# Optimization experiments

Hardware: AMD Instinct MI355X
Metric: run time of the kernel (lower is better)

The kernel has to match this reference:

```python
import jax, jax.numpy as jnp
import numpy as np

NU, NI, E, C = 100000, 50000, 500000, 128
TAU = 1.0
TEMP = 0.1

def _cos(a, b):
    # torch F.cosine_similarity: dot / (max(|a|,eps) * max(|b|,eps)), eps=1e-8
    na = jnp.maximum(jnp.linalg.norm(a, axis=-1), 1e-8)
    nb = jnp.maximum(jnp.linalg.norm(b, axis=-1), 1e-8)
    return jnp.sum(a * b, axis=-1) / (na * nb)

def _ln(x, g, b):
    m = jnp.mean(x, axis=-1, keepdims=True)
    v = jnp.var(x, axis=-1, keepdims=True)
    return (x - m) * jax.lax.rsqrt(v + 1e-5) * g + b

def _gumbel_hard(logits, u, tau):
    # F.gumbel_softmax(hard=True) with straight-through estimator; u ~ U(0,1) supplied as input
    g = -jnp.log(-jnp.log(u * (1.0 - 2e-6) + 1e-6))
    y = jax.nn.softmax((logits + g) / tau, axis=-1)
    hard = jax.nn.one_hot(jnp.argmax(y, axis=-1), y.shape[-1], dtype=y.dtype)
    return jax.lax.stop_gradient(hard - y) + y

def _forward(x_user, x_item, item_pop, u_user, u_item,
             Wu_proj, bu_proj, Wi_proj, bi_proj,
             Wu_enc, bu_enc, Wu_act, bu_act,
             Wi_enc, bi_enc, Wi_fair, bi_fair,
             Wl_ui, Wr_ui, b_ui, Wl_iu, Wr_iu, b_iu,
             ln_u_g, ln_u_b, ln_i_g, ln_i_b,
             edge_ui, edge_iu, user_neg_idx, item_neg_idx):
    hu = x_user @ Wu_proj + bu_proj          # [NU, C] user_proj
    hi = x_item @ Wi_proj + bi_proj          # [NI, C] item_proj
    # FairUserNet (fair_score head output is discarded in original; omitted)
    eu = jax.nn.relu(hu @ Wu_enc + bu_enc)
    action_logits = eu @ Wu_act + bu_act     # [NU, 2]
    # FairItemNet
    ei = jax.nn.relu(hi @ Wi_enc + bi_enc)
    pop = jax.nn.sigmoid(item_pop)[:, None]
    item_logits = jnp.concatenate([ei, pop], axis=-1) @ Wi_fair + bi_fair  # [NI, 2]
    user_probs = _gumbel_hard(action_logits, u_user, TAU)[:, 0]
    item_probs = _gumbel_hard(item_logits, u_item, TAU)[:, 0]  # WeightedSAGEConv discards edge weights
    del item_probs
    # structural contrastive loss over positive edges
    src, dst = edge_ui[0], edge_ui[1]
    ue, ie = hu[src], hi[dst]                # [E, C] gathers
    pos = _cos(ue, ie)
    neg = _cos(ue, hi[item_neg_idx]) + _cos(hu[user_neg_idx], ie)
    pe = jnp.exp(pos / TEMP)
    ne = jnp.exp(neg / TEMP)
    struct_loss = -jnp.mean(jnp.log(pe / (pe + ne)))
    # 3 hetero SAGE layers (2 hidden + final); aggr='add' (sum), lin_l bias, lin_r no bias
    isrc, idst = edge_iu[0], edge_iu[1]
    for l in range(3):
        agg_i = jax.ops.segment_sum(hu[src], dst, num_segments=NI)    # user -> item
        agg_u = jax.ops.segment_sum(hi[isrc], idst, num_segments=NU)  # item -> user
        new_i = agg_i @ Wl_ui[l] + b_ui[l] + hi @ Wr_ui[l]
        new_u = agg_u @ Wl_iu[l] + b_iu[l] + hu @ Wr_iu[l]
        if l < 2:  # LayerNorm + dropout(eval=identity) only on the 2 hidden layers
            new_u = _ln(new_u, ln_u_g[l], ln_u_b[l])
            new_i = _ln(new_i, ln_i_g[l], ln_i_b[l])
        hu, hi = new_u, new_i
    return hu, hi, struct_loss, user_probs

def setup_inputs():
    key = jax.random.key(0)
    ks = iter(jax.random.split(key, 64))
    def N(shape, s=1.0):
        return jax.random.normal(next(ks), shape, jnp.float32) * s
    def U(shape):
        return jax.random.uniform(next(ks), shape, dtype=jnp.float32)
    def I(shape, hi):
        return jax.random.randint(next(ks), shape, 0, hi, dtype=jnp.int32)
    w = 0.05
    users = I((E,), NU)
    items = I((E,), NI)
    return {
        'x_user': N((NU, C)), 'x_item': N((NI, C)),
        'item_pop': N((NI,)),
        'u_user': U((NU, 2)), 'u_item': U((NI, 2)),
        'Wu_proj': N((C, C), w), 'bu_proj': N((C,), w),
        'Wi_proj': N((C, C), w), 'bi_proj': N((C,), w),
        'Wu_enc': N((C, C), w), 'bu_enc': N((C,), w),
        'Wu_act': N((C, 2), w), 'bu_act': N((2,), w),
        'Wi_enc': N((C, C), w), 'bi_enc': N((C,), w),
        'Wi_fair': N((C + 1, 2), w), 'bi_fair': N((2,), w),
        'Wl_ui': N((3, C, C), w), 'Wr_ui': N((3, C, C), w), 'b_ui': N((3, C), w),
        'Wl_iu': N((3, C, C), w), 'Wr_iu': N((3, C, C), w), 'b_iu': N((3, C), w),
        'ln_u_g': jnp.ones((2, C), jnp.float32), 'ln_u_b': jnp.zeros((2, C), jnp.float32),
        'ln_i_g': jnp.ones((2, C), jnp.float32), 'ln_i_b': jnp.zeros((2, C), jnp.float32),
        'edge_ui': jnp.stack([users, items]),
        'edge_iu': jnp.stack([items, users]),
        'sensitive_attr': I((NU,), 2),
        'user_neg_idx': I((E,), NU),
        'item_neg_idx': I((E,), NI),
    }

def reference(x_user, x_item, item_pop, u_user, u_item,
              Wu_proj, bu_proj, Wi_proj, bi_proj,
              Wu_enc, bu_enc, Wu_act, bu_act,
              Wi_enc, bi_enc, Wi_fair, bi_fair,
              Wl_ui, Wr_ui, b_ui, Wl_iu, Wr_iu, b_iu,
              ln_u_g, ln_u_b, ln_i_g, ln_i_b,
              edge_ui, edge_iu, sensitive_attr, user_neg_idx, item_neg_idx):
    del sensitive_attr  # only feeds the discarded user fair_score head / .item() side effects
    return _forward(x_user, x_item, item_pop, u_user, u_item,
                    Wu_proj, bu_proj, Wi_proj, bi_proj,
                    Wu_enc, bu_enc, Wu_act, bu_act,
                    Wi_enc, bi_enc, Wi_fair, bi_fair,
                    Wl_ui, Wr_ui, b_ui, Wl_iu, Wr_iu, b_iu,
                    ln_u_g, ln_u_b, ln_i_g, ln_i_b,
                    edge_ui, edge_iu, user_neg_idx, item_neg_idx)
```

## Files before the change

kernel.cpp:

```cpp
#include <hip/hip_runtime.h>

#define NUU 100000
#define NII 50000
#define NEDGE 500000
#define NROWS (NII + NUU)

typedef float f32x4 __attribute__((ext_vector_type(4)));
typedef short bf16x8 __attribute__((ext_vector_type(8)));
typedef _Float16 half8v __attribute__((ext_vector_type(8)));
typedef _Float16 half4v __attribute__((ext_vector_type(4)));

struct GemmP {
    const float* A1; const unsigned short* Wh1; const unsigned short* Wl1;
    const float* A2; const unsigned short* Wh2; const unsigned short* Wl2;
    const float* bias; const float* lg; const float* lb;
    float* out; _Float16* out16; float* nrm; int M; int mode;
};

__global__ __launch_bounds__(256, 2)
void gemm_dual(GemmP P0, GemmP P1, int gb0,
               const float* __restrict__ pw, const float* __restrict__ pb,
               const float* __restrict__ pu, float* __restrict__ pout)
{
    const bool sel = (blockIdx.x >= gb0);
    const GemmP P = sel ? P1 : P0;
    const int bi = sel ? (int)blockIdx.x - gb0 : (int)blockIdx.x;
    const int tid = threadIdx.x;
    const int l  = tid & 63;
    const int w  = tid >> 6;
    const int lm = l & 15;
    const int lk = l >> 4;
    const int rowb = bi * 256 + w * 64;

    f32x4 acc[4][8];
#pragma unroll
    for (int mt = 0; mt < 4; ++mt)
#pragma unroll
        for (int nt = 0; nt < 8; ++nt) acc[mt][nt] = (f32x4){0.f, 0.f, 0.f, 0.f};

    const int nmat = (P.A2 != nullptr) ? 2 : 1;
    for (int m = 0; m < nmat; ++m) {
        const float* A = m ? P.A2 : P.A1;
        const unsigned short* Wh = m ? P.Wh2 : P.Wh1;
        const unsigned short* Wl = m ? P.Wl2 : P.Wl1;
#pragma unroll
        for (int kt = 0; kt < 4; ++kt) {
            bf16x8 ah[4], al[4];
#pragma unroll
            for (int mt = 0; mt < 4; ++mt) {
                int row = rowb + mt * 16 + lm;
                int rowc = row < P.M ? row : P.M - 1;
                const float* ap = A + (size_t)rowc * 128 + kt * 32 + lk * 8;
                float4 f0 = *(const float4*)ap;
                float4 f1 = *(const float4*)(ap + 4);
                float a8[8] = {f0.x, f0.y, f0.z, f0.w, f1.x, f1.y, f1.z, f1.w};
                union { bf16x8 v; unsigned int u[4]; } H, L;
#pragma unroll
                for (int p = 0; p < 4; ++p) {
                    unsigned int u0 = __float_as_uint(a8[2 * p]);
                    unsigned int u1 = __float_as_uint(a8[2 * p + 1]);
                    H.u[p] = (u0 >> 16) | (u1 & 0xffff0000u);
                    float l0 = a8[2 * p]     - __uint_as_float(u0 & 0xffff0000u);
                    float l1 = a8[2 * p + 1] - __uint_as_float(u1 & 0xffff0000u);
                    L.u[p] = (__float_as_uint(l0) >> 16) | (__float_as_uint(l1) & 0xffff0000u);
                }
                ah[mt] = H.v;
                al[mt] = L.v;
            }
#pragma unroll
            for (int h = 0; h < 2; ++h) {
                bf16x8 bh[4], bl[4];
#pragma unroll
                for (int q = 0; q < 4; ++q) {
                    size_t fo = (size_t)((kt * 8 + h * 4 + q) * 64 + l) * 8;
                    bh[q] = *(const bf16x8*)(Wh + fo);
                    bl[q] = *(const bf16x8*)(Wl + fo);
                }
#pragma unroll
                for (int mt = 0; mt < 4; ++mt)
#pragma unroll
                    for (int q = 0; q < 4; ++q) {
                        int nt = h * 4 + q;
                        acc[mt][nt] = __builtin_amdgcn_mfma_f32_16x16x32_bf16(bh[q], ah[mt], acc[mt][nt], 0, 0, 0);
                        acc[mt][nt] = __builtin_amdgcn_mfma_f32_16x16x32_bf16(bl[q], ah[mt], acc[mt][nt], 0, 0, 0);
                        acc[mt][nt] = __builtin_amdgcn_mfma_f32_16x16x32_bf16(bh[q], al[mt], acc[mt][nt], 0, 0, 0);
                    }
            }
        }
    }

    f32x4 bv[8];
#pragma unroll
    for (int nt = 0; nt < 8; ++nt)
        bv[nt] = *(const f32x4*)(P.bias + nt * 16 + lk * 4);

#pragma unroll
    for (int mt = 0; mt < 4; ++mt) {
        int row = rowb + mt * 16 + lm;
        bool valid = row < P.M;
        float v[8][4];
#pragma unroll
        for (int nt = 0; nt < 8; ++nt)
#pragma unroll
            for (int i = 0; i < 4; ++i) v[nt][i] = acc[mt][nt][i] + bv[nt][i];
        if (P.mode == 1) {
#pragma unroll
            for (int nt = 0; nt < 8; ++nt)
#pragma unroll
                for (int i = 0; i < 4; ++i) v[nt][i] = fmaxf(v[nt][i], 0.f);
        } else if (P.mode == 2) {
            float s = 0.f, sq = 0.f;
#pragma unroll
            for (int nt = 0; nt < 8; ++nt)
#pragma unroll
                for (int i = 0; i < 4; ++i) { s += v[nt][i]; sq += v[nt][i] * v[nt][i]; }
            s  += __shfl_xor(s, 16, 64);  s  += __shfl_xor(s, 32, 64);
            sq += __shfl_xor(sq, 16, 64); sq += __shfl_xor(sq, 32, 64);
            float mean = s * (1.f / 128.f);
            float var  = sq * (1.f / 128.f) - mean * mean;
            float inv  = rsqrtf(var + 1e-5f);
#pragma unroll
            for (int nt = 0; nt < 8; ++nt) {
                f32x4 lg = *(const f32x4*)(P.lg + nt * 16 + lk * 4);
                f32x4 lb = *(const f32x4*)(P.lb + nt * 16 + lk * 4);
#pragma unroll
                for (int i = 0; i < 4; ++i) v[nt][i] = (v[nt][i] - mean) * inv * lg[i] + lb[i];
            }
        }
        if (pout != nullptr) {
            float q0 = 0.f, q1 = 0.f;
#pragma unroll
            for (int nt = 0; nt < 8; ++nt) {
                const float* pp = pw + (size_t)(nt * 16 + lk * 4) * 2;
                f32x4 pa = *(const f32x4*)pp;
                f32x4 pc = *(const f32x4*)(pp + 4);
                q0 += v[nt][0] * pa[0] + v[nt][1] * pa[2] + v[nt][2] * pc[0] + v[nt][3] * pc[2];
                q1 += v[nt][0] * pa[1] + v[nt][1] * pa[3] + v[nt][2] * pc[1] + v[nt][3] * pc[3];
            }
            q0 += __shfl_xor(q0, 16, 64); q0 += __shfl_xor(q0, 32, 64);
            q1 += __shfl_xor(q1, 16, 64); q1 += __shfl_xor(q1, 32, 64);
            if (lk == 0 && valid) {
                float l0 = q0 + pb[0], l1 = q1 + pb[1];
                float u0 = pu[2 * row], u1 = pu[2 * row + 1];
                float g0 = -logf(-logf(u0 * (1.f - 2e-6f) + 1e-6f));
                float g1 = -logf(-logf(u1 * (1.f - 2e-6f) + 1e-6f));
                float z0 = l0 + g0, z1 = l1 + g1;
                float mz = fmaxf(z0, z1);
                float e0 = expf(z0 - mz), e1 = expf(z1 - mz);
                float y0 = e0 / (e0 + e1);
                pout[row] = (z0 >= z1) ? ((1.f - y0) + y0) : 0.f;
            }
        }
        if (P.nrm != nullptr) {
            float sq = 0.f;
#pragma unroll
            for (int nt = 0; nt < 8; ++nt)
#pragma unroll
                for (int i = 0; i < 4; ++i) sq += v[nt][i] * v[nt][i];
            sq += __shfl_xor(sq, 16, 64); sq += __shfl_xor(sq, 32, 64);
            if (lk == 0 && valid) P.nrm[row] = fmaxf(sqrtf(sq), 1e-8f);
        }
        if (valid) {
            if (P.out != nullptr) {
#pragma unroll
                for (int nt = 0; nt < 8; ++nt)
                    *(float4*)(P.out + (size_t)row * 128 + nt * 16 + lk * 4) =
                        make_float4(v[nt][0], v[nt][1], v[nt][2], v[nt][3]);
            }
            if (P.out16 != nullptr) {
#pragma unroll
                for (int nt = 0; nt < 8; ++nt) {
                    half4v h;
#pragma unroll
                    for (int i = 0; i < 4; ++i) h[i] = (_Float16)v[nt][i];
                    *(half4v*)(P.out16 + (size_t)row * 128 + nt * 16 + lk * 4) = h;
                }
            }
        }
    }
}

struct WSrc { const float* p[7]; };
__global__ void wsplit_k(WSrc S, unsigned short* __restrict__ wout)
{
    int gid = blockIdx.x * 256 + threadIdx.x;
    if (gid >= 15 * 16384) return;
    int m = gid >> 14;
    int idx = gid & 16383;
    int k = idx >> 7, n = idx & 127;
    const float* src;
    if (m == 0) src = S.p[0];
    else if (m == 1) src = S.p[1];
    else if (m == 2) src = S.p[2];
    else if (m < 6)  src = S.p[3] + (size_t)(m - 3) * 16384;
    else if (m < 9)  src = S.p[4] + (size_t)(m - 6) * 16384;
    else if (m < 12) src = S.p[5] + (size_t)(m - 9) * 16384;
    else             src = S.p[6] + (size_t)(m - 12) * 16384;
    float wv = src[idx];
    unsigned int u = __float_as_uint(wv);
    unsigned short hi = (unsigned short)(u >> 16);
    float lof = wv - __uint_as_float(u & 0xffff0000u);
    unsigned short lo = (unsigned short)(__float_as_uint(lof) >> 16);
    int kt = k >> 5, kr = k & 31;
    int dst = ((kt * 8 + (n >> 4)) * 64 + ((kr >> 3) * 16 + (n & 15))) * 8 + (kr & 7);
    unsigned short* wm = wout + (size_t)m * 32768;
    wm[dst] = hi;
    wm[dst + 16384] = lo;
}

__global__ void loss_k(const _Float16* __restrict__ hu16, const _Float16* __restrict__ hi16,
                       const float* __restrict__ nu, const float* __restrict__ ni,
                       const int* __restrict__ src, const int* __restrict__ dst,
                       const int* __restrict__ uneg, const int* __restrict__ ineg,
                       float* __restrict__ loss, int ne)
{
    __shared__ float ls[4];
    int lane = threadIdx.x & 63;
    int q = lane >> 4;
    int c8 = (lane & 15) * 8;
    int wib = threadIdx.x >> 6;
    int gw = (blockIdx.x * blockDim.x + threadIdx.x) >> 6;
    int nw = (gridDim.x * blockDim.x) >> 6;
    float part = 0.f;
    for (int eb = gw; eb < ne / 4; eb += nw) {
        int e = eb * 4 + q;
        int s = src[e], d = dst[e], un = uneg[e], in_ = ineg[e];
        half8v a = *(const half8v*)(hu16 + (size_t)s * 128 + c8);
        half8v b = *(const half8v*)(hi16 + (size_t)d * 128 + c8);
        half8v c = *(const half8v*)(hi16 + (size_t)in_ * 128 + c8);
        half8v dd = *(const half8v*)(hu16 + (size_t)un * 128 + c8);
        float p_sd = 0.f, p_sn = 0.f, p_nd = 0.f;
#pragma unroll
        for (int j = 0; j < 8; ++j) {
            float af = (float)a[j], bf = (float)b[j];
            p_sd += af * bf;
            p_sn += af * (float)c[j];
            p_nd += (float)dd[j] * bf;
        }
#pragma unroll
        for (int m = 1; m < 16; m <<= 1) {
            p_sd += __shfl_xor(p_sd, m, 64);
            p_sn += __shfl_xor(p_sn, m, 64);
            p_nd += __shfl_xor(p_nd, m, 64);
        }
        if ((lane & 15) == 0) {
            float pos = p_sd / (nu[s] * ni[d]);
            float neg = p_sn / (nu[s] * ni[in_]) + p_nd / (nu[un] * ni[d]);
            float pe = expf(pos * 10.f);
            float nex = expf(neg * 10.f);
            part += -logf(pe / (pe + nex));
        }
    }
    part += __shfl_xor(part, 16, 64);
    part += __shfl_xor(part, 32, 64);
    if (lane == 0) ls[wib] = part;
    __syncthreads();
    if (threadIdx.x == 0)
        atomicAdd(loss, (ls[0] + ls[1] + ls[2] + ls[3]) * (1.f / 500000.f));
}

__global__ void hist2_k(const int* __restrict__ ui_dst, const int* __restrict__ iu_dst,
                        int* __restrict__ deg)
{
    int e = blockIdx.x * blockDim.x + threadIdx.x;
    if (e < NEDGE) atomicAdd(&deg[ui_dst[e]], 1);
    else if (e < 2 * NEDGE) atomicAdd(&deg[NII + iu_dst[e - NEDGE]], 1);
}

__global__ void scan_part_k(const int* __restrict__ in, int* __restrict__ part, int N)
{
    __shared__ int wsum[4];
    int base = blockIdx.x * 1024 + threadIdx.x * 4;
    int s = 0;
    if (base + 3 < N) {
        int4 v = *(const int4*)(in + base);
        s = v.x + v.y + v.z + v.w;
    } else {
#pragma unroll
        for (int j = 0; j < 4; ++j) if (base + j < N) s += in[base + j];
    }
#pragma unroll
    for (int m = 1; m < 64; m <<= 1) s += __shfl_xor(s, m, 64);
    if ((threadIdx.x & 63) == 0) wsum[threadIdx.x >> 6] = s;
    __syncthreads();
    if (threadIdx.x == 0) part[blockIdx.x] = wsum[0] + wsum[1] + wsum[2] + wsum[3];
}

__global__ void scan_top_k(int* __restrict__ p, int nb)
{
    __shared__ int sm[256];
    int t = threadIdx.x;
    int v = (t < nb) ? p[t] : 0;
    sm[t] = v;
    __syncthreads();
    for (int o = 1; o < 256; o <<= 1) {
        int x = (t >= o) ? sm[t - o] : 0;
        __syncthreads();
        sm[t] += x;
        __syncthreads();
    }
    if (t < nb) p[t] = sm[t] - v;
}

__global__ void scan_final_k(const int* __restrict__ in, const int* __restrict__ part,
                             int* __restrict__ out, int N, int total)
{
    __shared__ int wtot[4];
    int tid = threadIdx.x;
    int lane = tid & 63, wid = tid >> 6;
    int base = blockIdx.x * 1024 + tid * 4;
    int v[4] = {0, 0, 0, 0};
    bool full = (base + 3 < N);
    if (full) {
        int4 q = *(const int4*)(in + base);
        v[0] = q.x; v[1] = q.y; v[2] = q.z; v[3] = q.w;
    } else {
#pragma unroll
        for (int j = 0; j < 4; ++j) if (base + j < N) v[j] = in[base + j];
    }
    int s = v[0] + v[1] + v[2] + v[3];
    int incl = s;
#pragma unroll
    for (int o = 1; o < 64; o <<= 1) {
        int n = __shfl_up(incl, o, 64);
        if (lane >= o) incl += n;
    }
    if (lane == 63) wtot[wid] = incl;
    __syncthreads();
    int woff = 0;
    for (int w2 = 0; w2 < wid; ++w2) woff += wtot[w2];
    int run = part[blockIdx.x] + woff + incl - s;
    if (full) {
        int4 o4 = make_int4(run, run + v[0], run + v[0] + v[1], run + v[0] + v[1] + v[2]);
        *(int4*)(out + base) = o4;
    } else {
#pragma unroll
        for (int j = 0; j < 4; ++j) {
            if (base + j < N) { out[base + j] = run; run += v[j]; }
        }
    }
    if (blockIdx.x == 0 && tid == 0) out[N] = total;
}

__global__ void fill2_k(const int* __restrict__ ui_dst, const int* __restrict__ ui_src,
                        const int* __restrict__ iu_dst, const int* __restrict__ iu_src,
                        const int* __restrict__ rowstart, int* __restrict__ cursor,
                        int* __restrict__ elist)
{
    int e = blockIdx.x * blockDim.x + threadIdx.x;
    if (e < NEDGE) {
        int d = ui_dst[e];
        int p = atomicAdd(&cursor[d], 1);
        elist[rowstart[d] + p] = ui_src[e];
    } else if (e < 2 * NEDGE) {
        int d = NII + iu_dst[e - NEDGE];
        int p = atomicAdd(&cursor[d], 1);
        elist[rowstart[d] + p] = iu_src[e - NEDGE];
    }
}

__global__ void agg_dual(const _Float16* __restrict__ hu16, const _Float16* __restrict__ hi16,
                         const int* __restrict__ rowstart, const int* __restrict__ elist,
                         float* __restrict__ hi_n, float* __restrict__ hu_n)
{
    int gt = blockIdx.x * blockDim.x + threadIdx.x;
    int w = gt >> 6, lane = gt & 63;
    if (w >= NROWS) return;
    const _Float16* src;
    float* dst;
    if (w < NII) { src = hu16; dst = hi_n + (size_t)w * 128; }
    else         { src = hi16; dst = hu_n + (size_t)(w - NII) * 128; }
    int q = lane >> 4;
    int c8 = (lane & 15) * 8;
    int s0 = rowstart[w], s1 = rowstart[w + 1];
    float a[8] = {0.f, 0.f, 0.f, 0.f, 0.f, 0.f, 0.f, 0.f};
    for (int e = s0 + q; e < s1; e += 4) {
        int s = elist[e];
        half8v v = *(const half8v*)(src + (size_t)s * 128 + c8);
#pragma unroll
        for (int j = 0; j < 8; ++j) a[j] += (float)v[j];
    }
#pragma unroll
    for (int j = 0; j < 8; ++j) {
        a[j] += __shfl_xor(a[j], 16, 64);
        a[j] += __shfl_xor(a[j], 32, 64);
    }
    if (lane < 16) {
        *(float4*)(dst + c8)     = make_float4(a[0], a[1], a[2], a[3]);
        *(float4*)(dst + c8 + 4) = make_float4(a[4], a[5], a[6], a[7]);
    }
}

extern "C" void kernel_launch(void* const* d_in, const int* in_sizes, int n_in,
                              void* d_out, int out_size, void* d_ws, size_t ws_size,
                              hipStream_t stream)
{
    const float* x_user  = (const float*)d_in[0];
    const float* x_item  = (const float*)d_in[1];
    const float* u_user  = (const float*)d_in[3];
    const float* Wu_proj = (const float*)d_in[5];
    const float* bu_proj = (const float*)d_in[6];
    const float* Wi_proj = (const float*)d_in[7];
    const float* bi_proj = (const float*)d_in[8];
    const float* Wu_enc  = (const float*)d_in[9];
    const float* bu_enc  = (const float*)d_in[10];
    const float* Wu_act  = (const float*)d_in[11];
    const float* bu_act  = (const float*)d_in[12];
    const float* Wl_ui = (const float*)d_in[17];
    const float* Wr_ui = (const float*)d_in[18];
    const float* b_ui  = (const float*)d_in[19];
    const float* Wl_iu = (const float*)d_in[20];
    const float* Wr_iu = (const float*)d_in[21];
    const float* b_iu  = (const float*)d_in[22];
    const float* ln_u_g = (const float*)d_in[23];
    const float* ln_u_b = (const float*)d_in[24];
    const float* ln_i_g = (const float*)d_in[25];
    const float* ln_i_b = (const float*)d_in[26];
    const int* edge_ui  = (const int*)d_in[27];
    const int* edge_iu  = (const int*)d_in[28];
    const int* user_neg = (const int*)d_in[30];
    const int* item_neg = (const int*)d_in[31];

    float* out = (float*)d_out;
    float* out_hu   = out;
    float* out_hi   = out + (size_t)NUU * 128;
    float* out_loss = out + 19200000;
    float* out_prob = out + 19200001;

    float* hu0  = (float*)d_ws;
    float* hi0  = hu0 + (size_t)NUU * 128;
    float* nu   = hi0 + (size_t)NII * 128;
    float* ni   = nu + NUU;
    int* ip   = (int*)(ni + NII);
    int* rs   = ip;  ip += NROWS + 16;
    int* cur  = ip;  ip += NROWS;
    int* el   = ip;  ip += 2 * NEDGE;
    int* pt   = ip;  ip += 160;
    unsigned short* wsp = (unsigned short*)ip;
    _Float16* hu16 = (_Float16*)(wsp + 15 * 32768);
    _Float16* hi16 = hu16 + (size_t)NUU * 128;

    const int* ui_src = edge_ui;
    const int* ui_dst = edge_ui + NEDGE;
    const int* iu_src = edge_iu;
    const int* iu_dst = edge_iu + NEDGE;

    const int GB_U = (NUU + 255) / 256, GB_I = (NII + 255) / 256;
    const int PB = (NROWS + 1023) / 1024;

    WSrc ws7 = {{Wu_proj, Wi_proj, Wu_enc, Wl_ui, Wr_ui, Wl_iu, Wr_iu}};
    wsplit_k<<<(15 * 16384 + 255) / 256, 256, 0, stream>>>(ws7, wsp);
    unsigned short* wm[15];
    for (int m = 0; m < 15; ++m) wm[m] = wsp + (size_t)m * 32768;

    GemmP pu_ = {x_user, wm[0], wm[0] + 16384, nullptr, nullptr, nullptr,
                 bu_proj, nullptr, nullptr, hu0, hu16, nu, NUU, 0};
    GemmP pi_ = {x_item, wm[1], wm[1] + 16384, nullptr, nullptr, nullptr,
                 bi_proj, nullptr, nullptr, hi0, hi16, ni, NII, 0};
    gemm_dual<<<GB_U + GB_I, 256, 0, stream>>>(pu_, pi_, GB_U, nullptr, nullptr, nullptr, nullptr);
    GemmP pe_ = {hu0, wm[2], wm[2] + 16384, nullptr, nullptr, nullptr,
                 bu_enc, nullptr, nullptr, nullptr, nullptr, nullptr, NUU, 1};
    gemm_dual<<<GB_U, 256, 0, stream>>>(pe_, pe_, GB_U, Wu_act, bu_act, u_user, out_prob);
    hipMemsetAsync(out_loss, 0, 4, stream);
    loss_k<<<2048, 256, 0, stream>>>(hu16, hi16, nu, ni, ui_src, ui_dst, user_neg, item_neg, out_loss, NEDGE);
    hipMemsetAsync(cur, 0, (size_t)NROWS * 4, stream);
    hist2_k<<<(2 * NEDGE + 255) / 256, 256, 0, stream>>>(ui_dst, iu_dst, cur);
    scan_part_k<<<PB, 256, 0, stream>>>(cur, pt, NROWS);
    scan_top_k<<<1, 256, 0, stream>>>(pt, PB);
    scan_final_k<<<PB, 256, 0, stream>>>(cur, pt, rs, NROWS, 2 * NEDGE);
    hipMemsetAsync(cur, 0, (size_t)NROWS * 4, stream);
    fill2_k<<<(2 * NEDGE + 255) / 256, 256, 0, stream>>>(ui_dst, ui_src, iu_dst, iu_src, rs, cur, el);

    float* hu_c = hu0; float* hi_c = hi0;
    float* hu_n = out_hu; float* hi_n = out_hi;
    for (int l = 0; l < 3; ++l) {
        int mode = (l < 2) ? 2 : 0;
        agg_dual<<<NROWS / 4, 256, 0, stream>>>(hu16, hi16, rs, el, hi_n, hu_n);
        GemmP li_ = {hi_n, wm[3 + l], wm[3 + l] + 16384, hi_c, wm[6 + l], wm[6 + l] + 16384,
                     b_ui + l * 128, ln_i_g + (l < 2 ? l : 0) * 128, ln_i_b + (l < 2 ? l : 0) * 128,
                     hi_n, (l < 2) ? hi16 : nullptr, nullptr, NII, mode};
        GemmP lu_ = {hu_n, wm[9 + l], wm[9 + l] + 16384, hu_c, wm[12 + l], wm[12 + l] + 16384,
                     b_iu + l * 128, ln_u_g + (l < 2 ? l : 0) * 128, ln_u_b + (l < 2 ? l : 0) * 128,
                     hu_n, (l < 2) ? hu16 : nullptr, nullptr, NUU, mode};
        gemm_dual<<<GB_I + GB_U, 256, 0, stream>>>(li_, lu_, GB_I, nullptr, nullptr, nullptr, nullptr);
        float* t;
        t = hu_c; hu_c = hu_n; hu_n = t;
        t = hi_c; hi_c = hi_n; hi_n = t;
    }
}
```

Measured before the change: 879.3 us.

## Keep SAGE layer activations in fp16 and raise gemm occupancy bound

The aggregation kernel now writes fp16 neighbour sums. The layer GEMMs read both the aggregate and the self term from fp16 buffers, and fp32 results are written only for the final layer's outputs. This cuts memory traffic for the intermediate [N,128] tensors and drops a workspace buffer. The GEMM launch bound is also raised from 2 to 3 blocks per CU. That trades register budget for occupancy and could cause spills. The self term and sums now carry fp16 rounding, which risks accuracy.

```diff
diff --git a/kernel.cpp b/kernel.cpp
--- a/kernel.cpp
+++ b/kernel.cpp
@@ -11,13 +11,13 @@
 typedef _Float16 half4v __attribute__((ext_vector_type(4)));
 
 struct GemmP {
-    const float* A1; const unsigned short* Wh1; const unsigned short* Wl1;
-    const float* A2; const unsigned short* Wh2; const unsigned short* Wl2;
+    const void* A1; const unsigned short* Wh1; const unsigned short* Wl1;
+    const void* A2; const unsigned short* Wh2; const unsigned short* Wl2;
     const float* bias; const float* lg; const float* lb;
-    float* out; _Float16* out16; float* nrm; int M; int mode;
+    float* out; _Float16* out16; float* nrm; int M; int mode; int a16;
 };
 
-__global__ __launch_bounds__(256, 2)
+__global__ __launch_bounds__(256, 3)
 void gemm_dual(GemmP P0, GemmP P1, int gb0,
                const float* __restrict__ pw, const float* __restrict__ pb,
                const float* __restrict__ pu, float* __restrict__ pout)
@@ -40,7 +40,7 @@
 
     const int nmat = (P.A2 != nullptr) ? 2 : 1;
     for (int m = 0; m < nmat; ++m) {
-        const float* A = m ? P.A2 : P.A1;
+        const void* A = m ? P.A2 : P.A1;
         const unsigned short* Wh = m ? P.Wh2 : P.Wh1;
         const unsigned short* Wl = m ? P.Wl2 : P.Wl1;
 #pragma unroll
@@ -50,10 +50,19 @@
             for (int mt = 0; mt < 4; ++mt) {
                 int row = rowb + mt * 16 + lm;
                 int rowc = row < P.M ? row : P.M - 1;
-                const float* ap = A + (size_t)rowc * 128 + kt * 32 + lk * 8;
-                float4 f0 = *(const float4*)ap;
-                float4 f1 = *(const float4*)(ap + 4);
-                float a8[8] = {f0.x, f0.y, f0.z, f0.w, f1.x, f1.y, f1.z, f1.w};
+                float a8[8];
+                if (P.a16) {
+                    const _Float16* ap = (const _Float16*)A + (size_t)rowc * 128 + kt * 32 + lk * 8;
+                    half8v hv = *(const half8v*)ap;
+#pragma unroll
+                    for (int j = 0; j < 8; ++j) a8[j] = (float)hv[j];
+                } else {
+                    const float* ap = (const float*)A + (size_t)rowc * 128 + kt * 32 + lk * 8;
+                    float4 f0 = *(const float4*)ap;
+                    float4 f1 = *(const float4*)(ap + 4);
+                    a8[0] = f0.x; a8[1] = f0.y; a8[2] = f0.z; a8[3] = f0.w;
+                    a8[4] = f1.x; a8[5] = f1.y; a8[6] = f1.z; a8[7] = f1.w;
+                }
                 union { bf16x8 v; unsigned int u[4]; } H, L;
 #pragma unroll
                 for (int p = 0; p < 4; ++p) {
@@ -361,15 +370,15 @@
 
 __global__ void agg_dual(const _Float16* __restrict__ hu16, const _Float16* __restrict__ hi16,
                          const int* __restrict__ rowstart, const int* __restrict__ elist,
-                         float* __restrict__ hi_n, float* __restrict__ hu_n)
+                         _Float16* __restrict__ ai16, _Float16* __restrict__ au16)
 {
     int gt = blockIdx.x * blockDim.x + threadIdx.x;
     int w = gt >> 6, lane = gt & 63;
     if (w >= NROWS) return;
     const _Float16* src;
-    float* dst;
-    if (w < NII) { src = hu16; dst = hi_n + (size_t)w * 128; }
-    else         { src = hi16; dst = hu_n + (size_t)(w - NII) * 128; }
+    _Float16* dst;
+    if (w < NII) { src = hu16; dst = ai16 + (size_t)w * 128; }
+    else         { src = hi16; dst = au16 + (size_t)(w - NII) * 128; }
     int q = lane >> 4;
     int c8 = (lane & 15) * 8;
     int s0 = rowstart[w], s1 = rowstart[w + 1];
@@ -386,8 +395,10 @@
         a[j] += __shfl_xor(a[j], 32, 64);
     }
     if (lane < 16) {
-        *(float4*)(dst + c8)     = make_float4(a[0], a[1], a[2], a[3]);
-        *(float4*)(dst + c8 + 4) = make_float4(a[4], a[5], a[6], a[7]);
+        half8v o;
+#pragma unroll
+        for (int j = 0; j < 8; ++j) o[j] = (_Float16)a[j];
+        *(half8v*)(dst + c8) = o;
     }
 }
 
@@ -427,18 +438,19 @@
     float* out_loss = out + 19200000;
     float* out_prob = out + 19200001;
 
-    float* hu0  = (float*)d_ws;
-    float* hi0  = hu0 + (size_t)NUU * 128;
-    float* nu   = hi0 + (size_t)NII * 128;
-    float* ni   = nu + NUU;
-    int* ip   = (int*)(ni + NII);
-    int* rs   = ip;  ip += NROWS + 16;
-    int* cur  = ip;  ip += NROWS;
-    int* el   = ip;  ip += 2 * NEDGE;
-    int* pt   = ip;  ip += 160;
+    float* hu0 = (float*)d_ws;
+    float* nu  = hu0 + (size_t)NUU * 128;
+    float* ni  = nu + NUU;
+    int* ip  = (int*)(ni + NII);
+    int* rs  = ip;  ip += NROWS + 16;
+    int* cur = ip;  ip += NROWS;
+    int* el  = ip;  ip += 2 * NEDGE;
+    int* pt  = ip;  ip += 160;
     unsigned short* wsp = (unsigned short*)ip;
     _Float16* hu16 = (_Float16*)(wsp + 15 * 32768);
     _Float16* hi16 = hu16 + (size_t)NUU * 128;
+    _Float16* au16 = hi16 + (size_t)NII * 128;
+    _Float16* ai16 = au16 + (size_t)NUU * 128;
 
     const int* ui_src = edge_ui;
     const int* ui_dst = edge_ui + NEDGE;
@@ -454,12 +466,12 @@
     for (int m = 0; m < 15; ++m) wm[m] = wsp + (size_t)m * 32768;
 
     GemmP pu_ = {x_user, wm[0], wm[0] + 16384, nullptr, nullptr, nullptr,
-                 bu_proj, nullptr, nullptr, hu0, hu16, nu, NUU, 0};
+                 bu_proj, nullptr, nullptr, hu0, hu16, nu, NUU, 0, 0};
     GemmP pi_ = {x_item, wm[1], wm[1] + 16384, nullptr, nullptr, nullptr,
-                 bi_proj, nullptr, nullptr, hi0, hi16, ni, NII, 0};
+                 bi_proj, nullptr, nullptr, nullptr, hi16, ni, NII, 0, 0};
     gemm_dual<<<GB_U + GB_I, 256, 0, stream>>>(pu_, pi_, GB_U, nullptr, nullptr, nullptr, nullptr);
     GemmP pe_ = {hu0, wm[2], wm[2] + 16384, nullptr, nullptr, nullptr,
-                 bu_enc, nullptr, nullptr, nullptr, nullptr, nullptr, NUU, 1};
+                 bu_enc, nullptr, nullptr, nullptr, nullptr, nullptr, NUU, 1, 0};
     gemm_dual<<<GB_U, 256, 0, stream>>>(pe_, pe_, GB_U, Wu_act, bu_act, u_user, out_prob);
     hipMemsetAsync(out_loss, 0, 4, stream);
     loss_k<<<2048, 256, 0, stream>>>(hu16, hi16, nu, ni, ui_src, ui_dst, user_neg, item_neg, out_loss, NEDGE);
@@ -471,20 +483,15 @@
     hipMemsetAsync(cur, 0, (size_t)NROWS * 4, stream);
     fill2_k<<<(2 * NEDGE + 255) / 256, 256, 0, stream>>>(ui_dst, ui_src, iu_dst, iu_src, rs, cur, el);
 
-    float* hu_c = hu0; float* hi_c = hi0;
-    float* hu_n = out_hu; float* hi_n = out_hi;
     for (int l = 0; l < 3; ++l) {
         int mode = (l < 2) ? 2 : 0;
-        agg_dual<<<NROWS / 4, 256, 0, stream>>>(hu16, hi16, rs, el, hi_n, hu_n);
-        GemmP li_ = {hi_n, wm[3 + l], wm[3 + l] + 16384, hi_c, wm[6 + l], wm[6 + l] + 16384,
+        agg_dual<<<NROWS / 4, 256, 0, stream>>>(hu16, hi16, rs, el, ai16, au16);
+        GemmP li_ = {ai16, wm[3 + l], wm[3 + l] + 16384, hi16, wm[6 + l], wm[6 + l] + 16384,
                      b_ui + l * 128, ln_i_g + (l < 2 ? l : 0) * 128, ln_i_b + (l < 2 ? l : 0) * 128,
-                     hi_n, (l < 2) ? hi16 : nullptr, nullptr, NII, mode};
-        GemmP lu_ = {hu_n, wm[9 + l], wm[9 + l] + 16384, hu_c, wm[12 + l], wm[12 + l] + 16384,
+                     (l == 2) ? out_hi : nullptr, (l < 2) ? hi16 : nullptr, nullptr, NII, mode, 1};
+        GemmP lu_ = {au16, wm[9 + l], wm[9 + l] + 16384, hu16, wm[12 + l], wm[12 + l] + 16384,
                      b_iu + l * 128, ln_u_g + (l < 2 ? l : 0) * 128, ln_u_b + (l < 2 ? l : 0) * 128,
-                     hu_n, (l < 2) ? hu16 : nullptr, nullptr, NUU, mode};
+                     (l == 2) ? out_hu : nullptr, (l < 2) ? hu16 : nullptr, nullptr, NUU, mode, 1};
         gemm_dual<<<GB_I + GB_U, 256, 0, stream>>>(li_, lu_, GB_I, nullptr, nullptr, nullptr, nullptr);
-        float* t;
-        t = hu_c; hu_c = hu_n; hu_n = t;
-        t = hi_c; hi_c = hi_n; hi_n = t;
-    }
-}
+    }
+}
```

New measurement: 1.186 ms. +34.8%, slower.
